# Kernel tuning notes

Hardware: AMD Instinct MI355X
Metric: run time of the kernel (lower is better)

Reference implementation:

```python
import jax, jax.numpy as jnp
import numpy as np

N_NODES = 100000


def _gcn_conv(x, edge_index, W, b, n):
    """PyG GCNConv: h = x @ W; add self-loops; symmetric deg^-1/2 norm; scatter-add; + b."""
    h = x @ W                                            # [N, F_out]
    src = jnp.concatenate([edge_index[0], jnp.arange(n)])  # self-loops appended
    dst = jnp.concatenate([edge_index[1], jnp.arange(n)])
    deg = jax.ops.segment_sum(jnp.ones_like(dst, dtype=h.dtype), dst, num_segments=n)
    dinv = jnp.where(deg > 0, jax.lax.rsqrt(deg), 0.0)   # deg^-1/2 with inf->0
    norm = dinv[src] * dinv[dst]                         # [E+N]
    msg = h[src] * norm[:, None]                         # gather + scale
    out = jax.ops.segment_sum(msg, dst, num_segments=n)  # scatter-add
    return out + b


def setup_inputs() -> dict:
    key = jax.random.key(0)
    ks = jax.random.split(key, 4)
    x = jax.random.normal(ks[0], (N_NODES, 128), dtype=jnp.float32)
    edge_index = jax.random.randint(ks[1], (2, 1600000), 0, N_NODES, dtype=jnp.int64)
    W1 = jax.random.normal(ks[2], (128, 128), dtype=jnp.float32) * (1.0 / np.sqrt(128))
    b1 = jnp.zeros((128,), dtype=jnp.float32)
    W2 = jax.random.normal(ks[3], (128, 16), dtype=jnp.float32) * (1.0 / np.sqrt(128))
    b2 = jnp.zeros((16,), dtype=jnp.float32)
    return {"x": x, "edge_index": edge_index, "W1": W1, "b1": b1, "W2": W2, "b2": b2}


def reference(x, edge_index, W1, b1, W2, b2):
    n = x.shape[0]
    h = jax.nn.relu(_gcn_conv(x, edge_index, W1, b1, n))
    out = _gcn_conv(h, edge_index, W2, b2, n)
    return out
```

## Files before the change

kernel.cpp:

```cpp
#include <hip/hip_runtime.h>
#include <hip/hip_bf16.h>

typedef __attribute__((ext_vector_type(8))) short bf16x8;
typedef __attribute__((ext_vector_type(4))) float f32x4;
typedef __attribute__((ext_vector_type(8))) unsigned short u16x8;

#define ELL_W 64
#define BSH   8
#define BCAP  4608
#define CHUNK 4096
#define PSPLIT 4


__device__ __forceinline__ float bf2f(unsigned short u) {
    return __uint_as_float(((unsigned int)u) << 16);
}
__device__ __forceinline__ unsigned short f2bf(float f) {
    unsigned int u = __float_as_uint(f);
    unsigned int r = (u + 0x7fffu + ((u >> 16) & 1u)) >> 16;
    return (unsigned short)r;
}
__device__ __forceinline__ int sel4(int sub, int4 v) {
    int s = (sub & 1) ? v.y : v.x;
    int t = (sub & 1) ? v.w : v.z;
    return (sub & 2) ? t : s;
}


__global__ void setup_kernel(int N, int NB, int* __restrict__ cursor, int* __restrict__ gcur,
                             const float* __restrict__ W1, unsigned short* __restrict__ wfrag) {
    int nb1 = (N + 255) >> 8;
    int nb2 = (NB * 16 + 255) >> 8;
    int b = blockIdx.x;
    if (b < nb1) {
        int i = b * 256 + threadIdx.x;
        if (i < N) cursor[i] = 0;
    } else if (b < nb1 + nb2) {
        int i = (b - nb1) * 256 + threadIdx.x;
        if (i < NB * 16) gcur[i] = 0;
    } else {
        int t = (b - nb1 - nb2) * 256 + threadIdx.x;
        if (t < 2048) {
            int ln = t & 63;
            int blk = t >> 6;
            int j = blk >> 2, k0 = blk & 3;
            int nn = ln & 15, cc = ln >> 4;
            int n = j * 16 + nn;
            unsigned short tmp[8];
#pragma unroll
            for (int i = 0; i < 8; ++i) {
                int k = k0 * 32 + cc * 8 + i;
                tmp[i] = f2bf(W1[(size_t)k * 128 + n]);
            }
            *(uint4*)&wfrag[(size_t)t * 8] = *(const uint4*)tmp;
        }
    }
}


__global__ __launch_bounds__(256) void p1_partition_kernel(const int* __restrict__ ei, int E, int N, int NB,
                                                           int* __restrict__ gcur, int* __restrict__ bucket) {
    __shared__ int hist[512];
    __shared__ int gbase[512];
    __shared__ int cur2[512];
    int tid = threadIdx.x;
    int c0 = blockIdx.x * CHUNK;

    for (int i = tid; i < NB; i += 256) { hist[i] = 0; cur2[i] = 0; }
    __syncthreads();

    int rec[16], bkt[16];
#pragma unroll
    for (int k = 0; k < 16; ++k) {
        int e = c0 + k * 256 + tid;
        int b = -1, r = 0;
        if (e < E) {
            int s = ei[e], d = ei[E + e];
            if ((unsigned)s < (unsigned)N && (unsigned)d < (unsigned)N) {
                b = d >> BSH;
                r = (s << BSH) | (d & ((1 << BSH) - 1));
            }
        }
        bkt[k] = b; rec[k] = r;
        if (b >= 0) atomicAdd(&hist[b], 1);
    }
    __syncthreads();

    for (int i = tid; i < NB; i += 256) {
        int c = hist[i];
        gbase[i] = (c > 0) ? atomicAdd(&gcur[i * 16], c) : 0;
    }
    __syncthreads();

#pragma unroll
    for (int k = 0; k < 16; ++k) {
        int b = bkt[k];
        if (b >= 0) {
            int r = atomicAdd(&cur2[b], 1);
            int pos = gbase[b] + r;
            if (pos < BCAP) bucket[(size_t)b * BCAP + pos] = rec[k];
        }
    }
}


__global__ __launch_bounds__(256) void p2_ell_kernel(const int* __restrict__ bucket,
                                                     const int* __restrict__ gcur, int N,
                                                     int* __restrict__ cursor, int* __restrict__ ell) {
    int b = blockIdx.x / PSPLIT;
    int seg = blockIdx.x % PSPLIT;
    int cnt = gcur[b * 16]; if (cnt > BCAP) cnt = BCAP;
    int per = (cnt + PSPLIT - 1) / PSPLIT;
    int k0 = seg * per;
    int k1 = min(k0 + per, cnt);
    const int* reg = &bucket[(size_t)b * BCAP];
    for (int k = k0 + threadIdx.x; k < k1; k += 256) {
        int rec = reg[k];
        int s = (int)(((unsigned)rec) >> BSH);
        int dst = (b << BSH) | (rec & ((1 << BSH) - 1));
        if (dst < N) {
            int pos = atomicAdd(&cursor[dst], 1);
            if (pos < ELL_W) ell[(size_t)dst * ELL_W + pos] = s;
        }
    }
}


__global__ void pad_dinv_kernel(const int* __restrict__ deg, int N,
                                int* __restrict__ ell, unsigned short* __restrict__ h1,
                                unsigned short* __restrict__ h2, float* __restrict__ dinv) {
    int i = blockIdx.x * blockDim.x + threadIdx.x;
    if (i < 128) h1[(size_t)N * 128 + i] = 0;
    if (i < 16) h2[(size_t)N * 16 + i] = 0;
    if (i < N) {
        int d = deg[i]; if (d > ELL_W) d = ELL_W;
        dinv[i] = rsqrtf((float)(deg[i] + 1));
        int d8 = (d + 7) & ~7; if (d8 > ELL_W) d8 = ELL_W;
        for (int k = d; k < d8; ++k) ell[(size_t)i * ELL_W + k] = N;
    }
}


__global__ __launch_bounds__(256) void gemm1_mfma_kernel(const float* __restrict__ X,
                                                         const unsigned short* __restrict__ wfrag,
                                                         const float* __restrict__ dinv,
                                                         unsigned short* __restrict__ H, int N) {
    __shared__ __align__(16) unsigned short wl[16384];
    int tid = threadIdx.x;
    {
        uint4* dst = (uint4*)wl;
        const uint4* src = (const uint4*)wfrag;
        for (int idx = tid; idx < 2048; idx += 256) dst[idx] = src[idx];
    }
    __syncthreads();

    int lane = tid & 63;
    int wave = tid >> 6;
    int m0 = blockIdx.x * 128 + wave * 32;
    int mrow = lane & 15;
    int kc = lane >> 4;

    f32x4 acc[2][8];
#pragma unroll
    for (int rt = 0; rt < 2; ++rt)
#pragma unroll
        for (int j = 0; j < 8; ++j) acc[rt][j] = (f32x4)(0.f);

#pragma unroll
    for (int k0 = 0; k0 < 4; ++k0) {
        bf16x8 a[2];
#pragma unroll
        for (int rt = 0; rt < 2; ++rt) {
            int row = m0 + rt * 16 + mrow;
            bf16x8 av = (bf16x8)(short)0;
            if (row < N) {
                const float4* p = (const float4*)&X[(size_t)row * 128 + k0 * 32 + kc * 8];
                float4 v0 = p[0], v1 = p[1];
                av[0] = (short)f2bf(v0.x); av[1] = (short)f2bf(v0.y);
                av[2] = (short)f2bf(v0.z); av[3] = (short)f2bf(v0.w);
                av[4] = (short)f2bf(v1.x); av[5] = (short)f2bf(v1.y);
                av[6] = (short)f2bf(v1.z); av[7] = (short)f2bf(v1.w);
            }
            a[rt] = av;
        }
#pragma unroll
        for (int j = 0; j < 8; ++j) {
            bf16x8 b = *(const bf16x8*)&wl[((size_t)(j * 4 + k0) * 64 + lane) * 8];
            acc[0][j] = __builtin_amdgcn_mfma_f32_16x16x32_bf16(a[0], b, acc[0][j], 0, 0, 0);
            acc[1][j] = __builtin_amdgcn_mfma_f32_16x16x32_bf16(a[1], b, acc[1][j], 0, 0, 0);
        }
    }

#pragma unroll
    for (int rt = 0; rt < 2; ++rt) {
#pragma unroll
        for (int r = 0; r < 4; ++r) {
            int row = m0 + rt * 16 + 4 * kc + r;
            if (row < N) {
                float dv = dinv[row];
#pragma unroll
                for (int j = 0; j < 8; ++j) {
                    H[(size_t)row * 128 + j * 16 + mrow] = f2bf(dv * acc[rt][j][r]);
                }
            }
        }
    }
}


__global__ __launch_bounds__(256) void agg128_fused_kernel(const unsigned short* __restrict__ H,
                                                           const int* __restrict__ ell,
                                                           const int* __restrict__ deg,
                                                           const float* __restrict__ dinv,
                                                           const float* __restrict__ b1,
                                                           const float* __restrict__ W2,
                                                           unsigned short* __restrict__ h2out, int N) {
    __shared__ float gbuf[4][128];
    int lane = threadIdx.x & 63;
    int w = threadIdx.x >> 6;
    int i0 = blockIdx.x * 16 + w * 4;

    int n = lane & 15;
    int q = lane >> 4;
    int sub = lane >> 4;
    int fl = lane & 15;

    float w2r[32];
#pragma unroll
    for (int m = 0; m < 32; ++m) {
        int mm = (m + 8 * q) & 31;
        w2r[m] = W2[(size_t)(q * 32 + mm) * 16 + n];
    }

    for (int nn = 0; nn < 4; ++nn) {
        int i = i0 + nn;
        if (i >= N) break;
        int d = deg[i]; if (d > ELL_W) d = ELL_W;
        int d8 = (d + 7) & ~7; if (d8 > ELL_W) d8 = ELL_W;
        float di = dinv[i];

        float a0, a1, a2, a3, a4, a5, a6, a7;
        {
            u16x8 hv = *(const u16x8*)&H[(size_t)i * 128 + 8 * fl];
            bool z = (sub != 0);
            a0 = z ? 0.f : bf2f(hv[0]); a1 = z ? 0.f : bf2f(hv[1]);
            a2 = z ? 0.f : bf2f(hv[2]); a3 = z ? 0.f : bf2f(hv[3]);
            a4 = z ? 0.f : bf2f(hv[4]); a5 = z ? 0.f : bf2f(hv[5]);
            a6 = z ? 0.f : bf2f(hv[6]); a7 = z ? 0.f : bf2f(hv[7]);
        }

        const int* row = &ell[(size_t)i * ELL_W];
        for (int e = 0; e < d8; e += 8) {
            int4 svA = *(const int4*)&row[e];
            int4 svB = *(const int4*)&row[e + 4];
            int sA = sel4(sub, svA);
            int sB = sel4(sub, svB);
            u16x8 gA = *(const u16x8*)&H[(size_t)sA * 128 + 8 * fl];
            u16x8 gB = *(const u16x8*)&H[(size_t)sB * 128 + 8 * fl];
            a0 += bf2f(gA[0]) + bf2f(gB[0]);
            a1 += bf2f(gA[1]) + bf2f(gB[1]);
            a2 += bf2f(gA[2]) + bf2f(gB[2]);
            a3 += bf2f(gA[3]) + bf2f(gB[3]);
            a4 += bf2f(gA[4]) + bf2f(gB[4]);
            a5 += bf2f(gA[5]) + bf2f(gB[5]);
            a6 += bf2f(gA[6]) + bf2f(gB[6]);
            a7 += bf2f(gA[7]) + bf2f(gB[7]);
        }

        a0 += __shfl_xor(a0, 32, 64); a0 += __shfl_xor(a0, 16, 64);
        a1 += __shfl_xor(a1, 32, 64); a1 += __shfl_xor(a1, 16, 64);
        a2 += __shfl_xor(a2, 32, 64); a2 += __shfl_xor(a2, 16, 64);
        a3 += __shfl_xor(a3, 32, 64); a3 += __shfl_xor(a3, 16, 64);
        a4 += __shfl_xor(a4, 32, 64); a4 += __shfl_xor(a4, 16, 64);
        a5 += __shfl_xor(a5, 32, 64); a5 += __shfl_xor(a5, 16, 64);
        a6 += __shfl_xor(a6, 32, 64); a6 += __shfl_xor(a6, 16, 64);
        a7 += __shfl_xor(a7, 32, 64); a7 += __shfl_xor(a7, 16, 64);

        if (sub == 0) {
            float4 bb0 = *(const float4*)&b1[8 * fl];
            float4 bb1 = *(const float4*)&b1[8 * fl + 4];
            float4 g0, g1;
            g0.x = fmaxf(di * a0 + bb0.x, 0.f);
            g0.y = fmaxf(di * a1 + bb0.y, 0.f);
            g0.z = fmaxf(di * a2 + bb0.z, 0.f);
            g0.w = fmaxf(di * a3 + bb0.w, 0.f);
            g1.x = fmaxf(di * a4 + bb1.x, 0.f);
            g1.y = fmaxf(di * a5 + bb1.y, 0.f);
            g1.z = fmaxf(di * a6 + bb1.z, 0.f);
            g1.w = fmaxf(di * a7 + bb1.w, 0.f);
            *(float4*)&gbuf[w][8 * fl] = g0;
            *(float4*)&gbuf[w][8 * fl + 4] = g1;
        }
        asm volatile("s_waitcnt lgkmcnt(0)" ::: "memory");

        float partial = 0.f;
#pragma unroll
        for (int t = 0; t < 8; ++t) {
            int off = (t * 4 + 8 * q) & 31;
            float4 gv = *(const float4*)&gbuf[w][q * 32 + off];
            partial += gv.x * w2r[t * 4 + 0] + gv.y * w2r[t * 4 + 1] +
                       gv.z * w2r[t * 4 + 2] + gv.w * w2r[t * 4 + 3];
        }
        partial += __shfl_xor(partial, 16, 64);
        partial += __shfl_xor(partial, 32, 64);
        if (lane < 16) h2out[(size_t)i * 16 + lane] = f2bf(di * partial);
    }
}


__global__ __launch_bounds__(256) void agg16_kernel(const unsigned short* __restrict__ H,
                                                    const int* __restrict__ ell,
                                                    const int* __restrict__ deg,
                                                    const float* __restrict__ dinv,
                                                    const float* __restrict__ b2,
                                                    float* __restrict__ out, int N) {
    int lane = threadIdx.x & 63;
    int i = blockIdx.x * 4 + (threadIdx.x >> 6);
    if (i >= N) return;
    int fl = lane & 7;
    int sub = lane >> 3;

    int d = deg[i]; if (d > ELL_W) d = ELL_W;
    int d8 = (d + 7) & ~7; if (d8 > ELL_W) d8 = ELL_W;
    float di = dinv[i];
    const int* row = &ell[(size_t)i * ELL_W];

    float a0, a1;
    {
        ushort2 hv = *(const ushort2*)&H[(size_t)i * 16 + 2 * fl];
        bool z = (sub != 0);
        a0 = z ? 0.f : bf2f(hv.x);
        a1 = z ? 0.f : bf2f(hv.y);
    }

    for (int e = 0; e < d8; e += 8) {
        int4 svA = *(const int4*)&row[e];
        int4 svB = *(const int4*)&row[e + 4];
        int sA_ = sel4(sub & 3, svA);
        int sB_ = sel4(sub & 3, svB);
        int s = (sub & 4) ? sB_ : sA_;
        ushort2 g = *(const ushort2*)&H[(size_t)s * 16 + 2 * fl];
        a0 += bf2f(g.x);
        a1 += bf2f(g.y);
    }

    a0 += __shfl_xor(a0, 32, 64); a0 += __shfl_xor(a0, 16, 64); a0 += __shfl_xor(a0, 8, 64);
    a1 += __shfl_xor(a1, 32, 64); a1 += __shfl_xor(a1, 16, 64); a1 += __shfl_xor(a1, 8, 64);

    if (lane < 8) {
        float2 o;
        o.x = di * a0 + b2[2 * fl];
        o.y = di * a1 + b2[2 * fl + 1];
        *(float2*)&out[(size_t)i * 16 + 2 * fl] = o;
    }
}


extern "C" void kernel_launch(void* const* d_in, const int* in_sizes, int n_in,
                              void* d_out, int out_size, void* d_ws, size_t ws_size,
                              hipStream_t stream) {
    const float* x = (const float*)d_in[0];
    const int* ei = (const int*)d_in[1];
    const float* W1 = (const float*)d_in[2];
    const float* b1 = (const float*)d_in[3];
    const float* W2 = (const float*)d_in[4];
    const float* b2 = (const float*)d_in[5];
    float* out = (float*)d_out;

    const int N = in_sizes[0] / 128;
    const int E = in_sizes[1] / 2;
    const int NB = (N + (1 << BSH) - 1) >> BSH;

    char* base = (char*)d_ws;
    size_t off = 0;
    auto align_up = [](size_t v) { return (v + 255) & ~(size_t)255; };

    int* cursor = (int*)(base + off);                      off = align_up(off + (size_t)N * 4);
    float* dinv = (float*)(base + off);                    off = align_up(off + (size_t)N * 4);
    int* ell = (int*)(base + off);                         off = align_up(off + (size_t)N * ELL_W * 4);
    int* gcur = (int*)(base + off);                        off = align_up(off + (size_t)NB * 16 * 4);
    int* bucket = (int*)(base + off);                      off = align_up(off + (size_t)NB * BCAP * 4);
    unsigned short* wfrag = (unsigned short*)(base + off); off = align_up(off + (size_t)16384 * 2);
    unsigned short* h1 = (unsigned short*)(base + off);    off = align_up(off + (size_t)(N + 1) * 128 * 2);
    unsigned short* h2 = (unsigned short*)(base + off);    off = align_up(off + (size_t)(N + 1) * 16 * 2);

    int nb1 = (N + 255) >> 8, nb2 = (NB * 16 + 255) >> 8;
    setup_kernel<<<nb1 + nb2 + 8, 256, 0, stream>>>(N, NB, cursor, gcur, W1, wfrag);

    int nchunks = (E + CHUNK - 1) / CHUNK;
    p1_partition_kernel<<<nchunks, 256, 0, stream>>>(ei, E, N, NB, gcur, bucket);
    p2_ell_kernel<<<NB * PSPLIT, 256, 0, stream>>>(bucket, gcur, N, cursor, ell);
    pad_dinv_kernel<<<(N + 255) / 256, 256, 0, stream>>>(cursor, N, ell, h1, h2, dinv);

    gemm1_mfma_kernel<<<(N + 127) / 128, 256, 0, stream>>>(x, wfrag, dinv, h1, N);
    agg128_fused_kernel<<<(N + 15) / 16, 256, 0, stream>>>(h1, ell, cursor, dinv, b1, W2, h2, N);
    agg16_kernel<<<(N + 3) / 4, 256, 0, stream>>>(h2, ell, cursor, dinv, b2, out, N);
}
```

Measured before the change: 213.7 us.

## Use smaller dst buckets with LDS cursors and fold degree/padding into ELL build

Halves the destination bucket size so each ELL-build block owns 128 destinations, counting their slots with shared-memory atomics instead of global atomics on a per-node cursor array. The degree, dinv and padding work from the separate pad kernel moves into the end of the ELL build, and the h1/h2 sentinel zeroing moves into setup. This removes one launch and the global cursor clear, at the cost of fewer blocks in the ELL build (no PSPLIT) and twice as many partition buckets with larger LDS histograms.

```diff
diff --git a/kernel.cpp b/kernel.cpp
--- a/kernel.cpp
+++ b/kernel.cpp
@@ -6,10 +6,10 @@
 typedef __attribute__((ext_vector_type(8))) unsigned short u16x8;
 
 #define ELL_W 64
-#define BSH   8
-#define BCAP  4608
+#define BSH   7
+#define BMSK  ((1 << BSH) - 1)
+#define BCAP  2432
 #define CHUNK 4096
-#define PSPLIT 4
 
 
 __device__ __forceinline__ float bf2f(unsigned short u) {
@@ -27,19 +27,16 @@
 }
 
 
-__global__ void setup_kernel(int N, int NB, int* __restrict__ cursor, int* __restrict__ gcur,
-                             const float* __restrict__ W1, unsigned short* __restrict__ wfrag) {
-    int nb1 = (N + 255) >> 8;
+__global__ void setup_kernel(int N, int NB, int* __restrict__ gcur,
+                             const float* __restrict__ W1, unsigned short* __restrict__ wfrag,
+                             unsigned short* __restrict__ h1, unsigned short* __restrict__ h2) {
     int nb2 = (NB * 16 + 255) >> 8;
     int b = blockIdx.x;
-    if (b < nb1) {
+    if (b < nb2) {
         int i = b * 256 + threadIdx.x;
-        if (i < N) cursor[i] = 0;
-    } else if (b < nb1 + nb2) {
-        int i = (b - nb1) * 256 + threadIdx.x;
         if (i < NB * 16) gcur[i] = 0;
-    } else {
-        int t = (b - nb1 - nb2) * 256 + threadIdx.x;
+    } else if (b < nb2 + 8) {
+        int t = (b - nb2) * 256 + threadIdx.x;
         if (t < 2048) {
             int ln = t & 63;
             int blk = t >> 6;
@@ -54,15 +51,18 @@
             }
             *(uint4*)&wfrag[(size_t)t * 8] = *(const uint4*)tmp;
         }
+    } else {
+        if (threadIdx.x < 128) h1[(size_t)N * 128 + threadIdx.x] = 0;
+        if (threadIdx.x < 16) h2[(size_t)N * 16 + threadIdx.x] = 0;
     }
 }
 
 
 __global__ __launch_bounds__(256) void p1_partition_kernel(const int* __restrict__ ei, int E, int N, int NB,
                                                            int* __restrict__ gcur, int* __restrict__ bucket) {
-    __shared__ int hist[512];
-    __shared__ int gbase[512];
-    __shared__ int cur2[512];
+    __shared__ int hist[1024];
+    __shared__ int gbase[1024];
+    __shared__ int cur2[1024];
     int tid = threadIdx.x;
     int c0 = blockIdx.x * CHUNK;
 
@@ -78,7 +78,7 @@
             int s = ei[e], d = ei[E + e];
             if ((unsigned)s < (unsigned)N && (unsigned)d < (unsigned)N) {
                 b = d >> BSH;
-                r = (s << BSH) | (d & ((1 << BSH) - 1));
+                r = (s << BSH) | (d & BMSK);
             }
         }
         bkt[k] = b; rec[k] = r;
@@ -106,37 +106,34 @@
 
 __global__ __launch_bounds__(256) void p2_ell_kernel(const int* __restrict__ bucket,
                                                      const int* __restrict__ gcur, int N,
-                                                     int* __restrict__ cursor, int* __restrict__ ell) {
-    int b = blockIdx.x / PSPLIT;
-    int seg = blockIdx.x % PSPLIT;
+                                                     int* __restrict__ deg, float* __restrict__ dinv,
+                                                     int* __restrict__ ell) {
+    __shared__ int lcur[128];
+    int b = blockIdx.x;
+    if (threadIdx.x < 128) lcur[threadIdx.x] = 0;
+    __syncthreads();
+
     int cnt = gcur[b * 16]; if (cnt > BCAP) cnt = BCAP;
-    int per = (cnt + PSPLIT - 1) / PSPLIT;
-    int k0 = seg * per;
-    int k1 = min(k0 + per, cnt);
     const int* reg = &bucket[(size_t)b * BCAP];
-    for (int k = k0 + threadIdx.x; k < k1; k += 256) {
+    for (int k = threadIdx.x; k < cnt; k += 256) {
         int rec = reg[k];
         int s = (int)(((unsigned)rec) >> BSH);
-        int dst = (b << BSH) | (rec & ((1 << BSH) - 1));
-        if (dst < N) {
-            int pos = atomicAdd(&cursor[dst], 1);
-            if (pos < ELL_W) ell[(size_t)dst * ELL_W + pos] = s;
-        }
-    }
-}
-
-
-__global__ void pad_dinv_kernel(const int* __restrict__ deg, int N,
-                                int* __restrict__ ell, unsigned short* __restrict__ h1,
-                                unsigned short* __restrict__ h2, float* __restrict__ dinv) {
-    int i = blockIdx.x * blockDim.x + threadIdx.x;
-    if (i < 128) h1[(size_t)N * 128 + i] = 0;
-    if (i < 16) h2[(size_t)N * 16 + i] = 0;
-    if (i < N) {
-        int d = deg[i]; if (d > ELL_W) d = ELL_W;
-        dinv[i] = rsqrtf((float)(deg[i] + 1));
-        int d8 = (d + 7) & ~7; if (d8 > ELL_W) d8 = ELL_W;
-        for (int k = d; k < d8; ++k) ell[(size_t)i * ELL_W + k] = N;
+        int dloc = rec & BMSK;
+        int pos = atomicAdd(&lcur[dloc], 1);
+        if (pos < ELL_W) ell[((size_t)(b << BSH) + dloc) * ELL_W + pos] = s;
+    }
+    __syncthreads();
+
+    if (threadIdx.x < 128) {
+        int i = (b << BSH) + threadIdx.x;
+        if (i < N) {
+            int d = lcur[threadIdx.x];
+            deg[i] = d;
+            dinv[i] = rsqrtf((float)(d + 1));
+            if (d > ELL_W) d = ELL_W;
+            int d8 = (d + 7) & ~7; if (d8 > ELL_W) d8 = ELL_W;
+            for (int k = d; k < d8; ++k) ell[(size_t)i * ELL_W + k] = N;
+        }
     }
 }
 
@@ -369,13 +366,13 @@
 
     const int N = in_sizes[0] / 128;
     const int E = in_sizes[1] / 2;
-    const int NB = (N + (1 << BSH) - 1) >> BSH;
+    const int NB = (N + BMSK) >> BSH;
 
     char* base = (char*)d_ws;
     size_t off = 0;
     auto align_up = [](size_t v) { return (v + 255) & ~(size_t)255; };
 
-    int* cursor = (int*)(base + off);                      off = align_up(off + (size_t)N * 4);
+    int* deg = (int*)(base + off);                         off = align_up(off + (size_t)N * 4);
     float* dinv = (float*)(base + off);                    off = align_up(off + (size_t)N * 4);
     int* ell = (int*)(base + off);                         off = align_up(off + (size_t)N * ELL_W * 4);
     int* gcur = (int*)(base + off);                        off = align_up(off + (size_t)NB * 16 * 4);
@@ -384,15 +381,14 @@
     unsigned short* h1 = (unsigned short*)(base + off);    off = align_up(off + (size_t)(N + 1) * 128 * 2);
     unsigned short* h2 = (unsigned short*)(base + off);    off = align_up(off + (size_t)(N + 1) * 16 * 2);
 
-    int nb1 = (N + 255) >> 8, nb2 = (NB * 16 + 255) >> 8;
-    setup_kernel<<<nb1 + nb2 + 8, 256, 0, stream>>>(N, NB, cursor, gcur, W1, wfrag);
+    int nb2 = (NB * 16 + 255) >> 8;
+    setup_kernel<<<nb2 + 9, 256, 0, stream>>>(N, NB, gcur, W1, wfrag, h1, h2);
 
     int nchunks = (E + CHUNK - 1) / CHUNK;
     p1_partition_kernel<<<nchunks, 256, 0, stream>>>(ei, E, N, NB, gcur, bucket);
-    p2_ell_kernel<<<NB * PSPLIT, 256, 0, stream>>>(bucket, gcur, N, cursor, ell);
-    pad_dinv_kernel<<<(N + 255) / 256, 256, 0, stream>>>(cursor, N, ell, h1, h2, dinv);
+    p2_ell_kernel<<<NB, 256, 0, stream>>>(bucket, gcur, N, deg, dinv, ell);
 
     gemm1_mfma_kernel<<<(N + 127) / 128, 256, 0, stream>>>(x, wfrag, dinv, h1, N);
-    agg128_fused_kernel<<<(N + 15) / 16, 256, 0, stream>>>(h1, ell, cursor, dinv, b1, W2, h2, N);
-    agg16_kernel<<<(N + 3) / 4, 256, 0, stream>>>(h2, ell, cursor, dinv, b2, out, N);
-}
+    agg128_fused_kernel<<<(N + 15) / 16, 256, 0, stream>>>(h1, ell, deg, dinv, b1, W2, h2, N);
+    agg16_kernel<<<(N + 3) / 4, 256, 0, stream>>>(h2, ell, deg, dinv, b2, out, N);
+}
```

Result: faster. 192.1 us (-10.1%).
